# Kernel tuning notes

Measured on AMD Instinct MI355X. Metric: run time of the kernel, lower is better.

## Reference

```python
import jax, jax.numpy as jnp
import numpy as np

B, S, D_IN, D_H, D_OUT, N_LAYERS = 16, 2048, 512, 1024, 10, 2


def setup_inputs() -> dict:
    key = jax.random.key(0)
    ks = jax.random.split(key, 12)
    s = lambda fan_in: 1.0 / np.sqrt(fan_in)
    return {
        "input_vec": jax.random.normal(ks[0], (B, S, D_IN), jnp.float32),
        "game_vector": jax.random.normal(ks[1], (B, N_LAYERS, D_H), jnp.float32),
        "user_vector": jax.random.normal(ks[2], (B, N_LAYERS, D_H), jnp.float32),
        # input_fc: Linear(D_IN, 2*D_IN) -> ReLU -> Linear(2*D_IN, D_H) -> ReLU
        "W1": jax.random.uniform(ks[3], (D_IN, 2 * D_IN), jnp.float32, -s(D_IN), s(D_IN)),
        "b1": jnp.zeros((2 * D_IN,), jnp.float32),
        "W2": jax.random.uniform(ks[4], (2 * D_IN, D_H), jnp.float32, -s(2 * D_IN), s(2 * D_IN)),
        "b2": jnp.zeros((D_H,), jnp.float32),
        # output_fc: Linear(D_H, D_H//2) -> ReLU -> Linear(D_H//2, D_OUT) -> LogSoftmax
        "W3": jax.random.uniform(ks[5], (D_H, D_H // 2), jnp.float32, -s(D_H), s(D_H)),
        "b3": jnp.zeros((D_H // 2,), jnp.float32),
        "W4": jax.random.uniform(ks[6], (D_H // 2, D_OUT), jnp.float32, -s(D_H // 2), s(D_H // 2)),
        "b4": jnp.zeros((D_OUT,), jnp.float32),
    }


def _causal_attention(h):
    # unscaled causal self-attention: softmax(h h^T + triu(-inf)) h
    scores = jnp.einsum("bsd,btd->bst", h, h)  # [B,S,S]
    seq = h.shape[1]
    causal = jnp.tril(jnp.ones((seq, seq), dtype=bool))
    scores = jnp.where(causal[None], scores, -jnp.inf)
    attn = jax.nn.softmax(scores, axis=-1)
    return jnp.einsum("bst,btd->bsd", attn, h)


def reference(input_vec, game_vector, user_vector, W1, b1, W2, b2, W3, b3, W4, b4):
    h = jax.nn.relu(input_vec @ W1 + b1)  # dropout is identity in eval
    h = jax.nn.relu(h @ W2 + b2)          # [B,S,D_H]
    ctx = _causal_attention(h)
    o = jax.nn.relu(ctx @ W3 + b3)
    out = jax.nn.log_softmax(o @ W4 + b4, axis=-1)
    return out, game_vector, user_vector
```

## Files before the change

### kernel.cpp

```cpp
#include <hip/hip_runtime.h>
#include <stdint.h>

#define B_   16
#define S_   2048
#define DIN  512
#define DH   1024
#define DOUT 10

typedef unsigned short u16;
typedef unsigned int   u32;

typedef __bf16 bf16_t;
typedef bf16_t bf16x8 __attribute__((ext_vector_type(8)));
typedef float  f32x4  __attribute__((ext_vector_type(4)));

#define MASKVAL (-3.0e4f)
#define PZ_U16 ((size_t)160 * 16384)

__device__ __forceinline__ float b2f(u16 u) {
    union { u32 i; float f; } v; v.i = ((u32)u) << 16; return v.f;
}
__device__ __forceinline__ u16 f2b(float f) {
    union { float f; u32 i; } v; v.f = f;
    u32 u = v.i;
    u32 r = (u + 0x7FFFu + ((u >> 16) & 1u)) >> 16;
    return (u16)r;
}
__device__ __forceinline__ u32 pack2(float a, float b) {
    return (u32)f2b(a) | ((u32)f2b(b) << 16);
}

__device__ __forceinline__ f32x4 mfma16(bf16x8 a, bf16x8 b, f32x4 c) {
    return __builtin_amdgcn_mfma_f32_16x16x32_bf16(a, b, c, 0, 0, 0);
}

__device__ __forceinline__ void load_lds16(const u16* g, u16* l) {
    __builtin_amdgcn_global_load_lds(
        (__attribute__((address_space(1))) u32*)(g),
        (__attribute__((address_space(3))) u32*)(l), 16, 0, 0);
}

template<bool F32>
__device__ __forceinline__ uint4 ld8(const void* base, size_t eidx) {
    if constexpr (F32) {
        const float* p = (const float*)base + eidx;
        float4 f0 = *(const float4*)p;
        float4 f1 = *(const float4*)(p + 4);
        uint4 r;
        r.x = pack2(f0.x, f0.y); r.y = pack2(f0.z, f0.w);
        r.z = pack2(f1.x, f1.y); r.w = pack2(f1.z, f1.w);
        return r;
    } else {
        return *(const uint4*)((const u16*)base + eidx);
    }
}

__global__ __launch_bounds__(256) void cvt_f32_bf16(
    const float* __restrict__ in, u16* __restrict__ out, int n8)
{
    int i = blockIdx.x * 256 + threadIdx.x;
    if (i >= n8) return;
    size_t e = (size_t)i * 8;
    float4 f0 = *(const float4*)(in + e);
    float4 f1 = *(const float4*)(in + e + 4);
    uint4 r;
    r.x = pack2(f0.x, f0.y); r.y = pack2(f0.z, f0.w);
    r.z = pack2(f1.x, f1.y); r.w = pack2(f1.z, f1.w);
    *(uint4*)(out + e) = r;
}

template<int QR>
__device__ __forceinline__ void rda(bf16x8 (&a)[4][2], const u16* T,
                                    int arow, int quad) {
#pragma unroll
    for (int mf = 0; mf < 4; ++mf) {
        const int row = arow + QR * 64 + mf * 16;
        const int sw = row & 7;
#pragma unroll
        for (int ks = 0; ks < 2; ++ks)
            a[mf][ks] = *(const bf16x8*)(T + row * 64 + (((ks * 4 + quad) ^ sw) << 3));
    }
}

template<int QC>
__device__ __forceinline__ void rdb(bf16x8 (&b)[2][2], const u16* T,
                                    int brow, int quad) {
#pragma unroll
    for (int nf = 0; nf < 2; ++nf) {
        const int row = brow + QC * 128 + nf * 16;
        const int sw = row & 7;
#pragma unroll
        for (int ks = 0; ks < 2; ++ks)
            b[nf][ks] = *(const bf16x8*)(T + row * 64 + (((ks * 4 + quad) ^ sw) << 3));
    }
}

template<int QR, int QC>
__device__ __forceinline__ void mmq(f32x4 (&acc)[2][2][4][2],
                                    const bf16x8 (&a)[4][2],
                                    const bf16x8 (&b)[2][2]) {
#pragma unroll
    for (int ks = 0; ks < 2; ++ks)
#pragma unroll
        for (int mf = 0; mf < 4; ++mf)
#pragma unroll
            for (int nf = 0; nf < 2; ++nf)
                acc[QR][QC][mf][nf] = mfma16(a[mf][ks], b[nf][ks], acc[QR][QC][mf][nf]);
}

#define G8BAR()  __builtin_amdgcn_s_barrier()
#define G8LGKM() do { asm volatile("s_waitcnt lgkmcnt(0)" ::: "memory"); \
                      __builtin_amdgcn_sched_barrier(0); } while (0)
#define G8VMC4() asm volatile("s_waitcnt vmcnt(4)" ::: "memory")

#define G8_LOOP_BODY(NT_)                                                     \
    const int NI = (NT_) >> 1;                                                \
    for (int i = 0; i < NI; ++i) {                                            \
        const int t1 = 2 * i + 1, t2 = 2 * i + 2, t3 = 2 * i + 3;             \
        rda<0>(a, AS_[0], arow, quad); rdb<0>(b0r, BS_[0], brow, quad);       \
        STGB(1, 2, t1); STGB(1, 3, t1);                                       \
        G8BAR(); G8LGKM();                                                    \
        __builtin_amdgcn_s_setprio(1); mmq<0, 0>(acc, a, b0r);                \
        __builtin_amdgcn_s_setprio(0); G8BAR();                               \
        rdb<1>(b1r, BS_[0], brow, quad);                                      \
        STGA(1, 1, t1); STGA(1, 3, t1);                                       \
        G8BAR(); G8LGKM();                                                    \
        __builtin_amdgcn_s_setprio(1); mmq<0, 1>(acc, a, b1r);                \
        __builtin_amdgcn_s_setprio(0); G8BAR();                               \
        rda<1>(a, AS_[0], arow, quad);                                        \
        if (t2 < (NT_)) { STGA(0, 0, t2); STGA(0, 2, t2); }                   \
        G8BAR(); G8LGKM();                                                    \
        __builtin_amdgcn_s_setprio(1); mmq<1, 0>(acc, a, b0r);                \
        __builtin_amdgcn_s_setprio(0); G8BAR();                               \
        if (t2 < (NT_)) { STGB(0, 0, t2); STGB(0, 1, t2); }                   \
        G8BAR();                                                              \
        __builtin_amdgcn_s_setprio(1); mmq<1, 1>(acc, a, b1r);                \
        __builtin_amdgcn_s_setprio(0);                                        \
        G8VMC4(); G8BAR();                                                    \
        rda<0>(a, AS_[1], arow, quad); rdb<0>(b0r, BS_[1], brow, quad);       \
        if (t2 < (NT_)) { STGB(0, 2, t2); STGB(0, 3, t2); }                   \
        G8BAR(); G8LGKM();                                                    \
        __builtin_amdgcn_s_setprio(1); mmq<0, 0>(acc, a, b0r);                \
        __builtin_amdgcn_s_setprio(0); G8BAR();                               \
        rdb<1>(b1r, BS_[1], brow, quad);                                      \
        if (t2 < (NT_)) { STGA(0, 1, t2); STGA(0, 3, t2); }                   \
        G8BAR(); G8LGKM();                                                    \
        __builtin_amdgcn_s_setprio(1); mmq<0, 1>(acc, a, b1r);                \
        __builtin_amdgcn_s_setprio(0); G8BAR();                               \
        rda<1>(a, AS_[1], arow, quad);                                        \
        if (t3 < (NT_)) { STGA(1, 0, t3); STGA(1, 2, t3); }                   \
        G8BAR(); G8LGKM();                                                    \
        __builtin_amdgcn_s_setprio(1); mmq<1, 0>(acc, a, b0r);                \
        __builtin_amdgcn_s_setprio(0); G8BAR();                               \
        if (t3 < (NT_)) { STGB(1, 0, t3); STGB(1, 1, t3); }                   \
        G8BAR();                                                              \
        __builtin_amdgcn_s_setprio(1); mmq<1, 1>(acc, a, b1r);                \
        __builtin_amdgcn_s_setprio(0);                                        \
        G8VMC4(); G8BAR();                                                    \
    }

__global__ __launch_bounds__(512, 2) void gemm8(
    const u16* __restrict__ A, const u16* __restrict__ Bt,
    const float* __restrict__ bias, u16* __restrict__ C,
    int N, int K, int do_relu)
{
    __shared__ __attribute__((aligned(16))) u16 AS_[2][16384];
    __shared__ __attribute__((aligned(16))) u16 BS_[2][16384];

    const int tid  = threadIdx.x;
    const int lane = tid & 63;
    const int w    = tid >> 6;
    const int wm   = w >> 2, wn = w & 3;
    const int quad = lane >> 4, l15 = lane & 15;
    const int m0 = blockIdx.x * 256, n0 = blockIdx.y * 256;

    const int rg = tid >> 3;
    const int ch = (lane & 7) ^ ((lane >> 3) & 7);
    const u16* gA = A  + (size_t)(m0 + rg) * K + ch * 8;
    const u16* gB = Bt + (size_t)(n0 + rg) * K + ch * 8;
    const int wslot = w * 512;

#define STGA(BUF, U, T) load_lds16(gA + (size_t)(U) * 64 * K + (T) * 64, \
                                   &AS_[BUF][(U) * 4096 + wslot])
#define STGB(BUF, U, T) load_lds16(gB + (size_t)(U) * 64 * K + (T) * 64, \
                                   &BS_[BUF][(U) * 4096 + wslot])

    f32x4 acc[2][2][4][2];
#pragma unroll
    for (int p = 0; p < 2; ++p)
#pragma unroll
    for (int q = 0; q < 2; ++q)
#pragma unroll
    for (int m = 0; m < 4; ++m)
#pragma unroll
    for (int n = 0; n < 2; ++n) acc[p][q][m][n] = (f32x4){0.f, 0.f, 0.f, 0.f};

    bf16x8 a[4][2], b0r[2][2], b1r[2][2];

    const int NT = K >> 6;

    STGA(0, 0, 0); STGA(0, 1, 0); STGA(0, 2, 0); STGA(0, 3, 0);
    STGB(0, 0, 0); STGB(0, 1, 0); STGB(0, 2, 0); STGB(0, 3, 0);
    STGA(1, 0, 1); STGA(1, 2, 1);
    STGB(1, 0, 1); STGB(1, 1, 1);
    G8VMC4(); G8BAR();

    const int arow = wm * 128 + l15;
    const int brow = wn * 32 + l15;
    G8_LOOP_BODY(NT)
#undef STGA
#undef STGB

    const int r0 = quad * 4;
#pragma unroll
    for (int qc = 0; qc < 2; ++qc)
#pragma unroll
    for (int nf = 0; nf < 2; ++nf) {
        const int col = n0 + qc * 128 + wn * 32 + nf * 16 + l15;
        const float bv = bias[col];
#pragma unroll
        for (int qr = 0; qr < 2; ++qr)
#pragma unroll
        for (int mf = 0; mf < 4; ++mf) {
            const int rowb = m0 + wm * 128 + qr * 64 + mf * 16 + r0;
#pragma unroll
            for (int r = 0; r < 4; ++r) {
                float v = acc[qr][qc][mf][nf][r] + bv;
                if (do_relu) v = fmaxf(v, 0.f);
                C[(size_t)(rowb + r) * N + col] = f2b(v);
            }
        }
    }
}

__global__ __launch_bounds__(512, 2) void score8(
    const u16* __restrict__ h, u16* __restrict__ P)
{
    __shared__ __attribute__((aligned(16))) u16 AS_[2][16384];
    __shared__ __attribute__((aligned(16))) u16 BS_[2][16384];

    const int z = blockIdx.x / 38;
    const int t = blockIdx.x % 38;

    if (t >= 36) {
        const int p = t - 36;
        const u16 mb = f2b(MASKVAL);
        const u32 m2 = (u32)mb | ((u32)mb << 16);
        uint4 mv; mv.x = m2; mv.y = m2; mv.z = m2; mv.w = m2;
        u16* Pz0 = P + (size_t)z * PZ_U16;
#pragma unroll
        for (int i = 0; i < 8; ++i) {
            const int idx = p * 8 + i;
            const int g  = idx >> 2;
            const int mi = 4 * g + ((idx >> 1) & 1);
            const int ni = 4 * g + 2 + (idx & 1);
            u16* Pz = Pz0 + (size_t)(4 * (g + 1) * (mi - 2 * g)) * 16384;
            const size_t rstride = (size_t)(4 * (g + 1)) * 128;
            for (int q = threadIdx.x; q < 2048; q += 512) {
                int row = q >> 4, cl = (q & 15) * 8;
                *(uint4*)&Pz[(size_t)row * rstride + ni * 128 + cl] = mv;
            }
        }
        return;
    }

    int bi = 0;
    while ((bi + 1) * (bi + 2) / 2 <= t) ++bi;
    const int bj = t - bi * (bi + 1) / 2;
    const bool diag = (bi == bj);

    const int tid  = threadIdx.x;
    const int lane = tid & 63;
    const int w    = tid >> 6;
    const int wm   = w >> 2, wn = w & 3;
    const int quad = lane >> 4, l15 = lane & 15;
    const int m0 = bi * 256, n0 = bj * 256;

    const u16* hz = h + (size_t)z * S_ * DH;
    const int rg = tid >> 3;
    const int ch = (lane & 7) ^ ((lane >> 3) & 7);
    const u16* gA = hz + (size_t)(m0 + rg) * DH + ch * 8;
    const u16* gB = hz + (size_t)(n0 + rg) * DH + ch * 8;
    const int wslot = w * 512;

#define STGA(BUF, U, T) load_lds16(gA + (size_t)(U) * 64 * DH + (T) * 64, \
                                   &AS_[BUF][(U) * 4096 + wslot])
#define STGB(BUF, U, T) load_lds16(gB + (size_t)(U) * 64 * DH + (T) * 64, \
                                   &BS_[BUF][(U) * 4096 + wslot])

    f32x4 acc[2][2][4][2];
#pragma unroll
    for (int p = 0; p < 2; ++p)
#pragma unroll
    for (int q = 0; q < 2; ++q)
#pragma unroll
    for (int m = 0; m < 4; ++m)
#pragma unroll
    for (int n = 0; n < 2; ++n) acc[p][q][m][n] = (f32x4){0.f, 0.f, 0.f, 0.f};

    bf16x8 a[4][2], b0r[2][2], b1r[2][2];

    const int NT = DH >> 6;

    STGA(0, 0, 0); STGA(0, 1, 0); STGA(0, 2, 0); STGA(0, 3, 0);
    STGB(0, 0, 0); STGB(0, 1, 0); STGB(0, 2, 0); STGB(0, 3, 0);
    STGA(1, 0, 1); STGA(1, 2, 1);
    STGB(1, 0, 1); STGB(1, 1, 1);
    G8VMC4(); G8BAR();

    const int arow = wm * 128 + l15;
    const int brow = wn * 32 + l15;
    G8_LOOP_BODY(NT)
#undef STGA
#undef STGB

    const int mi = 2 * bi + wm;
    const int g  = mi >> 2;
    u16* Pz = P + (size_t)z * PZ_U16
                + (size_t)(4 * (g + 1) * (mi - 2 * g)) * 16384;
    const size_t rstride = (size_t)(4 * (g + 1)) * 128;

    const int r0 = quad * 4;
#pragma unroll
    for (int qc = 0; qc < 2; ++qc) {
        const int ni = 2 * bj + qc;
#pragma unroll
        for (int nf = 0; nf < 2; ++nf) {
            const int cl = wn * 32 + nf * 16 + l15;
            const int colg = n0 + qc * 128 + cl;
#pragma unroll
            for (int qr = 0; qr < 2; ++qr)
#pragma unroll
            for (int mf = 0; mf < 4; ++mf) {
                const int rl = qr * 64 + mf * 16 + r0;
                const int rowg = m0 + wm * 128 + rl;
#pragma unroll
                for (int r = 0; r < 4; ++r) {
                    float v = acc[qr][qc][mf][nf][r];
                    if (diag && colg > rowg + r) v = MASKVAL;
                    Pz[(size_t)(rl + r) * rstride + ni * 128 + cl] = f2b(v);
                }
            }
        }
    }
}

__global__ __launch_bounds__(512, 2) void pv8(
    const u16* __restrict__ P, const u16* __restrict__ hT,
    u16* __restrict__ ctx, int nb)
{
    __shared__ __attribute__((aligned(16))) u16 AS_[2][16384];
    __shared__ __attribute__((aligned(16))) u16 BS_[2][16384];

    const int per_bi = 4 * nb;
    const int bi  = 7 - (int)(blockIdx.x / per_bi);
    const int rem = blockIdx.x % per_bi;
    const int nj  = rem & 3;
    const int z   = rem >> 2;

    const int g  = bi >> 1;
    const int K  = (g + 1) * 512;
    const int NT = K >> 6;
    const int n0 = nj * 256;

    const u16* Az = P + (size_t)z * PZ_U16
                      + (size_t)(4 * (g + 1) * (2 * bi - 2 * g)) * 16384;
    const u16* Bz = hT + (size_t)z * DH * S_;
    u16*       C  = ctx + (size_t)z * S_ * DH;

    const int tid  = threadIdx.x;
    const int lane = tid & 63;
    const int w    = tid >> 6;
    const int wm   = w >> 2, wn = w & 3;
    const int quad = lane >> 4, l15 = lane & 15;

    const int rg = tid >> 3;
    const int ch = (lane & 7) ^ ((lane >> 3) & 7);
    const u16* gA = Az + (size_t)rg * K + ch * 8;
    const u16* gB = Bz + (size_t)(n0 + rg) * S_ + ch * 8;
    const int wslot = w * 512;

#define STGA(BUF, U, T) load_lds16(gA + (size_t)(U) * 64 * K + (T) * 64, \
                                   &AS_[BUF][(U) * 4096 + wslot])
#define STGB(BUF, U, T) load_lds16(gB + (size_t)(U) * 64 * S_ + (T) * 64, \
                                   &BS_[BUF][(U) * 4096 + wslot])

    f32x4 acc[2][2][4][2];
#pragma unroll
    for (int p = 0; p < 2; ++p)
#pragma unroll
    for (int q = 0; q < 2; ++q)
#pragma unroll
    for (int m = 0; m < 4; ++m)
#pragma unroll
    for (int n = 0; n < 2; ++n) acc[p][q][m][n] = (f32x4){0.f, 0.f, 0.f, 0.f};

    bf16x8 a[4][2], b0r[2][2], b1r[2][2];

    STGA(0, 0, 0); STGA(0, 1, 0); STGA(0, 2, 0); STGA(0, 3, 0);
    STGB(0, 0, 0); STGB(0, 1, 0); STGB(0, 2, 0); STGB(0, 3, 0);
    STGA(1, 0, 1); STGA(1, 2, 1);
    STGB(1, 0, 1); STGB(1, 1, 1);
    G8VMC4(); G8BAR();

    const int arow = wm * 128 + l15;
    const int brow = wn * 32 + l15;
    G8_LOOP_BODY(NT)
#undef STGA
#undef STGB

    const int r0 = quad * 4;
#pragma unroll
    for (int qc = 0; qc < 2; ++qc)
#pragma unroll
    for (int nf = 0; nf < 2; ++nf) {
        const int col = n0 + qc * 128 + wn * 32 + nf * 16 + l15;
#pragma unroll
        for (int qr = 0; qr < 2; ++qr)
#pragma unroll
        for (int mf = 0; mf < 4; ++mf) {
            const int rowb = bi * 256 + wm * 128 + qr * 64 + mf * 16 + r0;
#pragma unroll
            for (int r = 0; r < 4; ++r)
                C[(size_t)(rowb + r) * DH + col] = f2b(acc[qr][qc][mf][nf][r]);
        }
    }
}

__global__ __launch_bounds__(256) void score_a(
    const u16* __restrict__ h, u16* __restrict__ P)
{
    __shared__ __attribute__((aligned(16))) u16 As[128 * 32];
    __shared__ __attribute__((aligned(16))) u16 Bs[128 * 32];

    const int mi = 15 - blockIdx.x;
    const int ni = blockIdx.y;
    const int g  = mi >> 2;
    const int r4 = (g + 1) * 4;
    if (ni >= r4) return;

    const int tid = threadIdx.x;
    u16* Pz = P + (size_t)blockIdx.z * PZ_U16
                + (size_t)(4 * (g + 1) * (mi - 2 * g)) * 16384;
    const size_t rstride = (size_t)r4 * 128;

    if (ni > mi) {
        const u16 mb = f2b(MASKVAL);
        const u32 m2 = (u32)mb | ((u32)mb << 16);
        uint4 mv; mv.x = m2; mv.y = m2; mv.z = m2; mv.w = m2;
#pragma unroll
        for (int i = 0; i < 8; ++i) {
            int q = tid + i * 256;
            int row = q >> 4, cl = (q & 15) * 8;
            *(uint4*)&Pz[(size_t)row * rstride + ni * 128 + cl] = mv;
        }
        return;
    }

    const int m0 = mi * 128, n0 = ni * 128;
    const u16* A = h + (size_t)blockIdx.z * S_ * DH;

    const int lane = tid & 63;
    const int w    = tid >> 6;
    const int wm   = w >> 1, wn = w & 1;
    const int quad = lane >> 4, l15 = lane & 15;

    const int c0 = tid, c1 = tid + 256;
    const u16* gA0 = A + ((size_t)(m0 + (c0 >> 2)) * DH + (c0 & 3) * 8);
    const u16* gA1 = A + ((size_t)(m0 + (c1 >> 2)) * DH + (c1 & 3) * 8);
    const u16* gB0 = A + ((size_t)(n0 + (c0 >> 2)) * DH + (c0 & 3) * 8);
    const u16* gB1 = A + ((size_t)(n0 + (c1 >> 2)) * DH + (c1 & 3) * 8);
    u16* lA0 = &As[(w * 64) * 8];
    u16* lA1 = &As[(256 + w * 64) * 8];
    u16* lB0 = &Bs[(w * 64) * 8];
    u16* lB1 = &Bs[(256 + w * 64) * 8];

    f32x4 acc[4][4];
#pragma unroll
    for (int i = 0; i < 4; ++i)
#pragma unroll
        for (int j = 0; j < 4; ++j) acc[i][j] = (f32x4){0.f, 0.f, 0.f, 0.f};

    const int nk = DH >> 5;
    for (int kk = 0; kk < nk; ++kk) {
        load_lds16(gA0, lA0); load_lds16(gA1, lA1);
        load_lds16(gB0, lB0); load_lds16(gB1, lB1);
        gA0 += 32; gA1 += 32; gB0 += 32; gB1 += 32;
        __syncthreads();
        bf16x8 af[4], bfr[4];
#pragma unroll
        for (int i = 0; i < 4; ++i)
            af[i] = *(const bf16x8*)&As[(wm * 64 + i * 16 + l15) * 32 + quad * 8];
#pragma unroll
        for (int j = 0; j < 4; ++j)
            bfr[j] = *(const bf16x8*)&Bs[(wn * 64 + j * 16 + l15) * 32 + quad * 8];
#pragma unroll
        for (int i = 0; i < 4; ++i)
#pragma unroll
            for (int j = 0; j < 4; ++j)
                acc[i][j] = mfma16(af[i], bfr[j], acc[i][j]);
        __syncthreads();
    }

    const int r0 = quad * 4;
#pragma unroll
    for (int j = 0; j < 4; ++j) {
        int cl = wn * 64 + j * 16 + l15;
#pragma unroll
        for (int i = 0; i < 4; ++i) {
            int rl = wm * 64 + i * 16 + r0;
#pragma unroll
            for (int r = 0; r < 4; ++r) {
                int row = rl + r;
                float v = (n0 + cl <= m0 + row) ? acc[i][j][r] : MASKVAL;
                Pz[(size_t)row * rstride + ni * 128 + cl] = f2b(v);
            }
        }
    }
}

__global__ __launch_bounds__(256) void softmax_rows(u16* __restrict__ P)
{
    const int tid = threadIdx.x;
    const int lane = tid & 63, w = tid >> 6;
    const size_t row = (size_t)blockIdx.x * 4 + w;
    const int z    = (int)(row >> 11);
    const int rloc = (int)(row & (S_ - 1));
    const int mi = rloc >> 7, g = mi >> 2;
    const int kb = g + 1;
    u16* p = P + (size_t)z * PZ_U16
               + (size_t)(4 * (g + 1) * (mi - 2 * g)) * 16384
               + (size_t)(rloc & 127) * ((g + 1) * 4 * 128);
    float v[32];
    float m = -1e30f;
    for (int k = 0; k < kb; ++k) {
        uint4 u = *(const uint4*)&p[k * 512 + lane * 8];
        const u32* uu = (const u32*)&u;
#pragma unroll
        for (int i = 0; i < 4; ++i) {
            float a = b2f((u16)(uu[i] & 0xFFFFu));
            float b = b2f((u16)(uu[i] >> 16));
            v[k * 8 + 2 * i] = a; v[k * 8 + 2 * i + 1] = b;
            m = fmaxf(m, fmaxf(a, b));
        }
    }
#pragma unroll
    for (int off = 32; off >= 1; off >>= 1) m = fmaxf(m, __shfl_xor(m, off, 64));
    float s = 0.f;
    for (int k = 0; k < kb; ++k)
#pragma unroll
        for (int i = 0; i < 8; ++i) {
            float e = __expf(v[k * 8 + i] - m);
            v[k * 8 + i] = e; s += e;
        }
#pragma unroll
    for (int off = 32; off >= 1; off >>= 1) s += __shfl_xor(s, off, 64);
    float inv = 1.0f / s;
    for (int k = 0; k < kb; ++k) {
        uint4 u; u32* uu = (u32*)&u;
#pragma unroll
        for (int i = 0; i < 4; ++i)
            uu[i] = pack2(v[k * 8 + 2 * i] * inv, v[k * 8 + 2 * i + 1] * inv);
        *(uint4*)&p[k * 512 + lane * 8] = u;
    }
}

__global__ __launch_bounds__(256) void pv_a(
    const u16* __restrict__ P, const u16* __restrict__ hT, u16* __restrict__ ctx,
    int nb)
{
    __shared__ __attribute__((aligned(16))) u16 As[128 * 32];
    __shared__ __attribute__((aligned(16))) u16 Bs[128 * 32];

    const int idx = blockIdx.x;
    const int per_mi = 8 * nb;
    const int mi = 15 - (idx / per_mi);
    const int sub = idx % per_mi;
    const int nblk = sub & 7;
    const int z    = sub >> 3;
    const int g = mi >> 2;
    const int m0 = mi * 128;
    const int n0 = nblk * 128;
    const size_t rstride = (size_t)((g + 1) * 4) * 128;
    const u16* A  = P  + (size_t)z * PZ_U16
                       + (size_t)(4 * (g + 1) * (mi - 2 * g)) * 16384;
    const u16* Bt = hT + (size_t)z * DH * S_;
    u16*      C   = ctx + (size_t)z * S_ * DH;

    const int tid  = threadIdx.x;
    const int lane = tid & 63;
    const int w    = tid >> 6;
    const int wm   = w >> 1, wn = w & 1;
    const int quad = lane >> 4, l15 = lane & 15;

    const int c0 = tid, c1 = tid + 256;
    const u16* gA0 = A  + ((size_t)(c0 >> 2) * rstride + (c0 & 3) * 8);
    const u16* gA1 = A  + ((size_t)(c1 >> 2) * rstride + (c1 & 3) * 8);
    const u16* gB0 = Bt + ((size_t)(n0 + (c0 >> 2)) * S_ + (c0 & 3) * 8);
    const u16* gB1 = Bt + ((size_t)(n0 + (c1 >> 2)) * S_ + (c1 & 3) * 8);
    u16* lA0 = &As[(w * 64) * 8];
    u16* lA1 = &As[(256 + w * 64) * 8];
    u16* lB0 = &Bs[(w * 64) * 8];
    u16* lB1 = &Bs[(256 + w * 64) * 8];

    f32x4 acc[4][4];
#pragma unroll
    for (int i = 0; i < 4; ++i)
#pragma unroll
        for (int j = 0; j < 4; ++j) acc[i][j] = (f32x4){0.f, 0.f, 0.f, 0.f};

    const int nk = (mi + 1) * 4;
    for (int kk = 0; kk < nk; ++kk) {
        load_lds16(gA0, lA0); load_lds16(gA1, lA1);
        load_lds16(gB0, lB0); load_lds16(gB1, lB1);
        gA0 += 32; gA1 += 32; gB0 += 32; gB1 += 32;
        __syncthreads();
        bf16x8 af[4], bfr[4];
#pragma unroll
        for (int i = 0; i < 4; ++i)
            af[i] = *(const bf16x8*)&As[(wm * 64 + i * 16 + l15) * 32 + quad * 8];
#pragma unroll
        for (int j = 0; j < 4; ++j)
            bfr[j] = *(const bf16x8*)&Bs[(wn * 64 + j * 16 + l15) * 32 + quad * 8];
#pragma unroll
        for (int i = 0; i < 4; ++i)
#pragma unroll
            for (int j = 0; j < 4; ++j)
                acc[i][j] = mfma16(af[i], bfr[j], acc[i][j]);
        __syncthreads();
    }

    const int r0 = quad * 4;
#pragma unroll
    for (int j = 0; j < 4; ++j) {
        int col = n0 + wn * 64 + j * 16 + l15;
#pragma unroll
        for (int i = 0; i < 4; ++i) {
            int rowb = m0 + wm * 64 + i * 16 + r0;
#pragma unroll
            for (int r = 0; r < 4; ++r)
                C[(size_t)(rowb + r) * DH + col] = f2b(acc[i][j][r]);
        }
    }
}

template<bool AF32>
__global__ __launch_bounds__(256) void gemm_bt_bias_relu(
    const void* __restrict__ A, const u16* __restrict__ Bt,
    const float* __restrict__ bias, u16* __restrict__ C,
    int M, int N, int K, int do_relu)
{
    __shared__ __attribute__((aligned(16))) u16 As[128 * 32];
    __shared__ __attribute__((aligned(16))) u16 Bs[128 * 32];

    const int tid  = threadIdx.x;
    const int lane = tid & 63;
    const int w    = tid >> 6;
    const int wm   = w >> 1, wn = w & 1;
    const int quad = lane >> 4, l15 = lane & 15;

    const int m0 = blockIdx.x * 128;
    const int n0 = blockIdx.y * 128;

    const int c0 = tid, c1 = tid + 256;
    size_t eA0 = (size_t)(m0 + (c0 >> 2)) * K + (c0 & 3) * 8;
    size_t eA1 = (size_t)(m0 + (c1 >> 2)) * K + (c1 & 3) * 8;
    size_t eB0 = (size_t)(n0 + (c0 >> 2)) * K + (c0 & 3) * 8;
    size_t eB1 = (size_t)(n0 + (c1 >> 2)) * K + (c1 & 3) * 8;

    f32x4 acc[4][4];
#pragma unroll
    for (int i = 0; i < 4; ++i)
#pragma unroll
        for (int j = 0; j < 4; ++j) acc[i][j] = (f32x4){0.f, 0.f, 0.f, 0.f};

    uint4 va0 = ld8<AF32>(A, eA0), va1 = ld8<AF32>(A, eA1);
    uint4 vb0 = ld8<false>(Bt, eB0), vb1 = ld8<false>(Bt, eB1);

    const int nk = K >> 5;
    for (int kk = 0; kk < nk; ++kk) {
        __syncthreads();
        *(uint4*)&As[c0 * 8] = va0;
        *(uint4*)&As[c1 * 8] = va1;
        *(uint4*)&Bs[c0 * 8] = vb0;
        *(uint4*)&Bs[c1 * 8] = vb1;
        if (kk + 1 < nk) {
            eA0 += 32; eA1 += 32; eB0 += 32; eB1 += 32;
            va0 = ld8<AF32>(A, eA0); va1 = ld8<AF32>(A, eA1);
            vb0 = ld8<false>(Bt, eB0); vb1 = ld8<false>(Bt, eB1);
        }
        __syncthreads();
        bf16x8 af[4], bfr[4];
#pragma unroll
        for (int i = 0; i < 4; ++i)
            af[i] = *(const bf16x8*)&As[(wm * 64 + i * 16 + l15) * 32 + quad * 8];
#pragma unroll
        for (int j = 0; j < 4; ++j)
            bfr[j] = *(const bf16x8*)&Bs[(wn * 64 + j * 16 + l15) * 32 + quad * 8];
#pragma unroll
        for (int i = 0; i < 4; ++i)
#pragma unroll
            for (int j = 0; j < 4; ++j)
                acc[i][j] = mfma16(af[i], bfr[j], acc[i][j]);
    }

    const int r0 = quad * 4;
#pragma unroll
    for (int j = 0; j < 4; ++j) {
        int col = n0 + wn * 64 + j * 16 + l15;
        float bv = bias[col];
#pragma unroll
        for (int i = 0; i < 4; ++i) {
            int rowb = m0 + wm * 64 + i * 16 + r0;
#pragma unroll
            for (int r = 0; r < 4; ++r) {
                float v = acc[i][j][r] + bv;
                if (do_relu) v = fmaxf(v, 0.f);
                C[(size_t)(rowb + r) * N + col] = f2b(v);
            }
        }
    }
}

__global__ __launch_bounds__(256) void transpose_cvt(
    const float* __restrict__ in, u16* __restrict__ out, int R, int C)
{
    __shared__ u16 t[32][33];
    int c0 = blockIdx.x * 32, r0 = blockIdx.y * 32;
    int tx = threadIdx.x, ty = threadIdx.y;
#pragma unroll
    for (int i = 0; i < 4; ++i)
        t[ty + i * 8][tx] = f2b(in[(size_t)(r0 + ty + i * 8) * C + c0 + tx]);
    __syncthreads();
#pragma unroll
    for (int i = 0; i < 4; ++i)
        out[(size_t)(c0 + ty + i * 8) * R + r0 + tx] = t[tx][ty + i * 8];
}

__global__ __launch_bounds__(256) void transpose_b(
    const u16* __restrict__ in, u16* __restrict__ out, int R, int C)
{
    __shared__ u16 t[32][33];
    const u16* ip = in  + (size_t)blockIdx.z * R * C;
    u16*       op = out + (size_t)blockIdx.z * R * C;
    int c0 = blockIdx.x * 32, r0 = blockIdx.y * 32;
    int tx = threadIdx.x, ty = threadIdx.y;
#pragma unroll
    for (int i = 0; i < 4; ++i)
        t[ty + i * 8][tx] = ip[(size_t)(r0 + ty + i * 8) * C + c0 + tx];
    __syncthreads();
#pragma unroll
    for (int i = 0; i < 4; ++i)
        op[(size_t)(c0 + ty + i * 8) * R + r0 + tx] = t[tx][ty + i * 8];
}

__global__ __launch_bounds__(256) void head_logsoftmax(
    const u16* __restrict__ o, const float* __restrict__ W4,
    const float* __restrict__ b4, float* __restrict__ out)
{
    __shared__ float W4s[DIN * DOUT];
    __shared__ float b4s[DOUT];
    const int tid = threadIdx.x;
    for (int i = tid; i < DIN * DOUT; i += 256) W4s[i] = W4[i];
    if (tid < DOUT) b4s[tid] = b4[tid];
    __syncthreads();
    const int lane = tid & 63, w = tid >> 6;
    const size_t row = (size_t)blockIdx.x * 4 + w;
    const uint4 ov = *(const uint4*)&o[row * DIN + lane * 8];
    const u32* ou = (const u32*)&ov;
    float oc[8];
#pragma unroll
    for (int i = 0; i < 4; ++i) {
        oc[2*i]   = b2f((u16)(ou[i] & 0xFFFFu));
        oc[2*i+1] = b2f((u16)(ou[i] >> 16));
    }
    float acc[DOUT];
#pragma unroll
    for (int c = 0; c < DOUT; ++c) acc[c] = 0.f;
#pragma unroll
    for (int i = 0; i < 8; ++i) {
        int k = lane * 8 + i;
        float x = oc[i];
#pragma unroll
        for (int c = 0; c < DOUT; ++c) acc[c] += x * W4s[k * DOUT + c];
    }
#pragma unroll
    for (int off = 32; off >= 1; off >>= 1)
#pragma unroll
        for (int c = 0; c < DOUT; ++c) acc[c] += __shfl_xor(acc[c], off, 64);
    float mx = -1e30f;
#pragma unroll
    for (int c = 0; c < DOUT; ++c) { acc[c] += b4s[c]; mx = fmaxf(mx, acc[c]); }
    float sum = 0.f;
#pragma unroll
    for (int c = 0; c < DOUT; ++c) sum += __expf(acc[c] - mx);
    float lse = mx + logf(sum);
    if (lane == 0) {
#pragma unroll
        for (int c = 0; c < DOUT; ++c) out[row * DOUT + c] = acc[c] - lse;
    }
}

extern "C" void kernel_launch(void* const* d_in, const int* in_sizes, int n_in,
                              void* d_out, int out_size, void* d_ws, size_t ws_size,
                              hipStream_t stream) {
    const float* x  = (const float*)d_in[0];
    const float* gv = (const float*)d_in[1];
    const float* uv = (const float*)d_in[2];
    const float* W1 = (const float*)d_in[3];
    const float* b1 = (const float*)d_in[4];
    const float* W2 = (const float*)d_in[5];
    const float* b2 = (const float*)d_in[6];
    const float* W3 = (const float*)d_in[7];
    const float* b3 = (const float*)d_in[8];
    const float* W4 = (const float*)d_in[9];
    const float* b4 = (const float*)d_in[10];
    float* out = (float*)d_out;

    char* ws = (char*)d_ws;
    const size_t MB64 = (size_t)67108864;
    const size_t MiB  = (size_t)1048576;
    const size_t TIER_A3 = 2 * MB64 + 80 * MiB + 4 * MiB;
    const size_t TIER_A2 = 2 * MB64 + 72 * MiB + 8 * MiB;
    const size_t TIER_B  = 3 * MB64 + 5 * MiB;

    if (ws_size >= TIER_A3) {
        u16* h1  = (u16*)(ws);
        u16* hT  = h1;
        u16* h   = (u16*)(ws + MB64);
        u16* ctx = h;
        u16* xb  = (u16*)(ws + 2 * MB64);
        u16* P   = xb;
        u16* o   = xb;
        u16* W1t = (u16*)(ws + 2 * MB64 + 80 * MiB);
        u16* W2t = W1t + 512 * 1024;
        u16* W3t = W2t + 1024 * 1024;

        cvt_f32_bf16<<<8192, 256, 0, stream>>>(x, xb, 2097152);
        transpose_cvt<<<dim3(32, 16), dim3(32, 8), 0, stream>>>(W1, W1t, 512, 1024);
        transpose_cvt<<<dim3(32, 32), dim3(32, 8), 0, stream>>>(W2, W2t, 1024, 1024);
        transpose_cvt<<<dim3(16, 32), dim3(32, 8), 0, stream>>>(W3, W3t, 1024, 512);

        gemm8<<<dim3(128, 4), 512, 0, stream>>>(xb, W1t, b1, h1, 1024, 512, 1);
        gemm8<<<dim3(128, 4), 512, 0, stream>>>(h1, W2t, b2, h,  1024, 1024, 1);

        transpose_b<<<dim3(32, 64, 16), dim3(32, 8), 0, stream>>>(h, hT, 2048, 1024);
        score8<<<38 * 16, 512, 0, stream>>>(h, P);
        softmax_rows<<<8192, 256, 0, stream>>>(P);
        pv8<<<32 * 16, 512, 0, stream>>>(P, hT, ctx, 16);

        gemm8<<<dim3(128, 2), 512, 0, stream>>>(ctx, W3t, b3, o, 512, 1024, 1);
        head_logsoftmax<<<8192, 256, 0, stream>>>(o, W4, b4, out);
    } else if (ws_size >= TIER_A2) {
        u16* h1   = (u16*)(ws);
        u16* ctx  = h1;
        u16* h    = (u16*)(ws + MB64);
        u16* o    = h;
        u16* xb   = (u16*)(ws + 2 * MB64);
        u16* hT_c = xb;
        u16* P_c  = (u16*)(ws + 2 * MB64 + 32 * MiB);
        u16* W1t  = (u16*)(ws + 2 * MB64 + 72 * MiB);
        u16* W2t  = W1t + 512 * 1024;
        u16* W3t  = W2t + 1024 * 1024;

        cvt_f32_bf16<<<8192, 256, 0, stream>>>(x, xb, 2097152);
        transpose_cvt<<<dim3(32, 16), dim3(32, 8), 0, stream>>>(W1, W1t, 512, 1024);
        transpose_cvt<<<dim3(32, 32), dim3(32, 8), 0, stream>>>(W2, W2t, 1024, 1024);
        transpose_cvt<<<dim3(16, 32), dim3(32, 8), 0, stream>>>(W3, W3t, 1024, 512);

        gemm8<<<dim3(128, 4), 512, 0, stream>>>(xb, W1t, b1, h1, 1024, 512, 1);
        gemm8<<<dim3(128, 4), 512, 0, stream>>>(h1, W2t, b2, h,  1024, 1024, 1);

        for (int c = 0; c < 2; ++c) {
            const u16* hc  = h   + (size_t)c * 8 * S_ * DH;
            u16*       cxc = ctx + (size_t)c * 8 * S_ * DH;
            transpose_b<<<dim3(32, 64, 8), dim3(32, 8), 0, stream>>>(hc, hT_c, 2048, 1024);
            score8<<<38 * 8, 512, 0, stream>>>(hc, P_c);
            softmax_rows<<<4096, 256, 0, stream>>>(P_c);
            pv_a<<<16 * 8 * 8, 256, 0, stream>>>(P_c, hT_c, cxc, 8);
        }

        gemm8<<<dim3(128, 2), 512, 0, stream>>>(ctx, W3t, b3, o, 512, 1024, 1);
        head_logsoftmax<<<8192, 256, 0, stream>>>(o, W4, b4, out);
    } else if (ws_size >= TIER_B) {
        u16* h1   = (u16*)(ws);
        u16* ctx  = h1;
        u16* h    = (u16*)(ws + MB64);
        u16* xb   = (u16*)(ws + 2 * MB64);
        u16* hT_c = xb;
        u16* P_c  = (u16*)(ws + 2 * MB64 + 16 * MiB);
        u16* o    = (u16*)(ws + 2 * MB64);
        u16* W1t  = (u16*)(ws + 3 * MB64);
        u16* W2t  = W1t + 512 * 1024;
        u16* W3t  = W2t + 1024 * 1024;

        cvt_f32_bf16<<<8192, 256, 0, stream>>>(x, xb, 2097152);
        transpose_cvt<<<dim3(32, 16), dim3(32, 8), 0, stream>>>(W1, W1t, 512, 1024);
        transpose_cvt<<<dim3(32, 32), dim3(32, 8), 0, stream>>>(W2, W2t, 1024, 1024);
        transpose_cvt<<<dim3(16, 32), dim3(32, 8), 0, stream>>>(W3, W3t, 1024, 512);

        gemm8<<<dim3(128, 4), 512, 0, stream>>>(xb, W1t, b1, h1, 1024, 512, 1);
        gemm8<<<dim3(128, 4), 512, 0, stream>>>(h1, W2t, b2, h,  1024, 1024, 1);

        for (int c = 0; c < 4; ++c) {
            const u16* hc  = h   + (size_t)c * 4 * S_ * DH;
            u16*       cxc = ctx + (size_t)c * 4 * S_ * DH;
            transpose_b<<<dim3(32, 64, 4), dim3(32, 8), 0, stream>>>(hc, hT_c, 2048, 1024);
            score8<<<38 * 4, 512, 0, stream>>>(hc, P_c);
            softmax_rows<<<2048, 256, 0, stream>>>(P_c);
            pv_a<<<16 * 8 * 4, 256, 0, stream>>>(P_c, hT_c, cxc, 4);
        }

        gemm8<<<dim3(128, 2), 512, 0, stream>>>(ctx, W3t, b3, o, 512, 1024, 1);
        head_logsoftmax<<<8192, 256, 0, stream>>>(o, W4, b4, out);
    } else {
        u16* h    = (u16*)(ws);
        u16* hT_b = (u16*)(ws + MB64);
        u16* P_b  = (u16*)(ws + MB64 + 4 * MiB);
        u16* ctx_b= (u16*)(ws + MB64 + 12 * MiB);
        u16* o_b  = (u16*)(ws + MB64 + 16 * MiB);
        u16* W1t  = (u16*)(ws + MB64 + 18 * MiB);
        u16* W2t  = W1t + 512 * 1024;
        u16* W3t  = W2t + 1024 * 1024;
        u16* h1_b = P_b;

        transpose_cvt<<<dim3(32, 16), dim3(32, 8), 0, stream>>>(W1, W1t, 512, 1024);
        transpose_cvt<<<dim3(32, 32), dim3(32, 8), 0, stream>>>(W2, W2t, 1024, 1024);
        transpose_cvt<<<dim3(16, 32), dim3(32, 8), 0, stream>>>(W3, W3t, 1024, 512);

        for (int c = 0; c < 8; ++c) {
            const float* xc = x + (size_t)c * 4096 * DIN;
            u16*         hc = h + (size_t)c * 4096 * DH;
            gemm_bt_bias_relu<true ><<<dim3(32, 8), 256, 0, stream>>>(xc, W1t, b1, h1_b,
                                                                      4096, 1024, 512, 1);
            gemm_bt_bias_relu<false><<<dim3(32, 8), 256, 0, stream>>>(h1_b, W2t, b2, hc,
                                                                      4096, 1024, 1024, 1);
        }
        for (int b = 0; b < B_; ++b) {
            const u16* hb = h + (size_t)b * S_ * DH;
            transpose_b<<<dim3(32, 64, 1), dim3(32, 8), 0, stream>>>(hb, hT_b, 2048, 1024);
            score_a<<<dim3(16, 16, 1), 256, 0, stream>>>(hb, P_b);
            softmax_rows<<<512, 256, 0, stream>>>(P_b);
            pv_a<<<16 * 8, 256, 0, stream>>>(P_b, hT_b, ctx_b, 1);
            gemm_bt_bias_relu<false><<<dim3(16, 4), 256, 0, stream>>>(ctx_b, W3t, b3, o_b,
                                                                      2048, 512, 1024, 1);
            head_logsoftmax<<<512, 256, 0, stream>>>(o_b, W4, b4,
                                                     out + (size_t)b * S_ * DOUT);
        }
    }

    size_t n_gv = (size_t)in_sizes[1], n_uv = (size_t)in_sizes[2];
    size_t o0 = (size_t)out_size - n_gv - n_uv;
    hipMemcpyAsync(out + o0,        gv, n_gv * 4, hipMemcpyDeviceToDevice, stream);
    hipMemcpyAsync(out + o0 + n_gv, uv, n_uv * 4, hipMemcpyDeviceToDevice, stream);
}
```

Measured before the change: 588.4 us.

## Vectorize h transpose, merge weight prep, XCD-remap score blocks, batch head rows

Several independent tweaks. The three weight transpose-convert launches are merged into one wprep kernel. The bf16 h transpose now uses 16-byte vector loads and stores over 64x32 tiles. score8 remaps block indices so blocks of the same batch land on the same XCD when the batch count is a multiple of eight. head_logsoftmax processes four rows per wave, so it launches a quarter as many blocks and amortizes its W4 shared-memory load. The aim is fewer launches, better memory coalescing and better L2 locality, at the cost of more bank conflicts in the new transpose's shared-memory access pattern.

```diff
diff --git a/kernel.cpp b/kernel.cpp
--- a/kernel.cpp
+++ b/kernel.cpp
@@ -234,13 +234,20 @@
 }
 
 __global__ __launch_bounds__(512, 2) void score8(
-    const u16* __restrict__ h, u16* __restrict__ P)
+    const u16* __restrict__ h, u16* __restrict__ P, int nbb)
 {
     __shared__ __attribute__((aligned(16))) u16 AS_[2][16384];
     __shared__ __attribute__((aligned(16))) u16 BS_[2][16384];
 
-    const int z = blockIdx.x / 38;
-    const int t = blockIdx.x % 38;
+    int z, t;
+    if ((nbb & 7) == 0) {
+        const int xcd = blockIdx.x & 7, slot = blockIdx.x >> 3;
+        z = (slot / 38) * 8 + xcd;
+        t = slot % 38;
+    } else {
+        z = blockIdx.x / 38;
+        t = blockIdx.x % 38;
+    }
 
     if (t >= 36) {
         const int p = t - 36;
@@ -722,36 +729,51 @@
     }
 }
 
-__global__ __launch_bounds__(256) void transpose_cvt(
-    const float* __restrict__ in, u16* __restrict__ out, int R, int C)
+__global__ __launch_bounds__(256) void wprep(
+    const float* __restrict__ W1, const float* __restrict__ W2,
+    const float* __restrict__ W3,
+    u16* __restrict__ W1t, u16* __restrict__ W2t, u16* __restrict__ W3t)
 {
     __shared__ u16 t[32][33];
-    int c0 = blockIdx.x * 32, r0 = blockIdx.y * 32;
-    int tx = threadIdx.x, ty = threadIdx.y;
-#pragma unroll
-    for (int i = 0; i < 4; ++i)
-        t[ty + i * 8][tx] = f2b(in[(size_t)(r0 + ty + i * 8) * C + c0 + tx]);
+    int i = blockIdx.x;
+    const float* in; u16* out; int R, C, xt;
+    if (i < 512)       { in = W1; out = W1t; R = 512;  C = 1024; xt = 32; }
+    else if (i < 1536) { in = W2; out = W2t; R = 1024; C = 1024; xt = 32; i -= 512; }
+    else               { in = W3; out = W3t; R = 1024; C = 512;  xt = 16; i -= 1536; }
+    const int c0 = (i % xt) * 32, r0 = (i / xt) * 32;
+    const int tx = threadIdx.x, ty = threadIdx.y;
+#pragma unroll
+    for (int k = 0; k < 4; ++k)
+        t[ty + k * 8][tx] = f2b(in[(size_t)(r0 + ty + k * 8) * C + c0 + tx]);
     __syncthreads();
 #pragma unroll
-    for (int i = 0; i < 4; ++i)
-        out[(size_t)(c0 + ty + i * 8) * R + r0 + tx] = t[tx][ty + i * 8];
-}
-
-__global__ __launch_bounds__(256) void transpose_b(
+    for (int k = 0; k < 4; ++k)
+        out[(size_t)(c0 + ty + k * 8) * R + r0 + tx] = t[tx][ty + k * 8];
+}
+
+__global__ __launch_bounds__(256) void transpose_v(
     const u16* __restrict__ in, u16* __restrict__ out, int R, int C)
 {
-    __shared__ u16 t[32][33];
+    __shared__ u16 st[64][33];
     const u16* ip = in  + (size_t)blockIdx.z * R * C;
     u16*       op = out + (size_t)blockIdx.z * R * C;
-    int c0 = blockIdx.x * 32, r0 = blockIdx.y * 32;
-    int tx = threadIdx.x, ty = threadIdx.y;
-#pragma unroll
-    for (int i = 0; i < 4; ++i)
-        t[ty + i * 8][tx] = ip[(size_t)(r0 + ty + i * 8) * C + c0 + tx];
+    const int c0 = blockIdx.x * 64, r0 = blockIdx.y * 32;
+    const int t = threadIdx.x;
+    {
+        const int row = t >> 3, ch = t & 7;
+        uint4 v = *(const uint4*)&ip[(size_t)(r0 + row) * C + c0 + ch * 8];
+        const u16* pv = (const u16*)&v;
+#pragma unroll
+        for (int k = 0; k < 8; ++k) st[ch * 8 + k][row] = pv[k];
+    }
     __syncthreads();
-#pragma unroll
-    for (int i = 0; i < 4; ++i)
-        op[(size_t)(c0 + ty + i * 8) * R + r0 + tx] = t[tx][ty + i * 8];
+    {
+        const int oc = t >> 2, r4 = t & 3;
+        uint4 v; u16* pv = (u16*)&v;
+#pragma unroll
+        for (int k = 0; k < 8; ++k) pv[k] = st[oc][r4 * 8 + k];
+        *(uint4*)&op[(size_t)(c0 + oc) * R + r0 + r4 * 8] = v;
+    }
 }
 
 __global__ __launch_bounds__(256) void head_logsoftmax(
@@ -765,39 +787,41 @@
     if (tid < DOUT) b4s[tid] = b4[tid];
     __syncthreads();
     const int lane = tid & 63, w = tid >> 6;
-    const size_t row = (size_t)blockIdx.x * 4 + w;
-    const uint4 ov = *(const uint4*)&o[row * DIN + lane * 8];
-    const u32* ou = (const u32*)&ov;
-    float oc[8];
-#pragma unroll
-    for (int i = 0; i < 4; ++i) {
-        oc[2*i]   = b2f((u16)(ou[i] & 0xFFFFu));
-        oc[2*i+1] = b2f((u16)(ou[i] >> 16));
-    }
-    float acc[DOUT];
-#pragma unroll
-    for (int c = 0; c < DOUT; ++c) acc[c] = 0.f;
-#pragma unroll
-    for (int i = 0; i < 8; ++i) {
-        int k = lane * 8 + i;
-        float x = oc[i];
-#pragma unroll
-        for (int c = 0; c < DOUT; ++c) acc[c] += x * W4s[k * DOUT + c];
-    }
-#pragma unroll
-    for (int off = 32; off >= 1; off >>= 1)
-#pragma unroll
-        for (int c = 0; c < DOUT; ++c) acc[c] += __shfl_xor(acc[c], off, 64);
-    float mx = -1e30f;
-#pragma unroll
-    for (int c = 0; c < DOUT; ++c) { acc[c] += b4s[c]; mx = fmaxf(mx, acc[c]); }
-    float sum = 0.f;
-#pragma unroll
-    for (int c = 0; c < DOUT; ++c) sum += __expf(acc[c] - mx);
-    float lse = mx + logf(sum);
-    if (lane == 0) {
-#pragma unroll
-        for (int c = 0; c < DOUT; ++c) out[row * DOUT + c] = acc[c] - lse;
+    for (int rr = 0; rr < 4; ++rr) {
+        const size_t row = (size_t)blockIdx.x * 16 + w * 4 + rr;
+        const uint4 ov = *(const uint4*)&o[row * DIN + lane * 8];
+        const u32* ou = (const u32*)&ov;
+        float oc[8];
+#pragma unroll
+        for (int i = 0; i < 4; ++i) {
+            oc[2*i]   = b2f((u16)(ou[i] & 0xFFFFu));
+            oc[2*i+1] = b2f((u16)(ou[i] >> 16));
+        }
+        float acc[DOUT];
+#pragma unroll
+        for (int c = 0; c < DOUT; ++c) acc[c] = 0.f;
+#pragma unroll
+        for (int i = 0; i < 8; ++i) {
+            int k = lane * 8 + i;
+            float x = oc[i];
+#pragma unroll
+            for (int c = 0; c < DOUT; ++c) acc[c] += x * W4s[k * DOUT + c];
+        }
+#pragma unroll
+        for (int off = 32; off >= 1; off >>= 1)
+#pragma unroll
+            for (int c = 0; c < DOUT; ++c) acc[c] += __shfl_xor(acc[c], off, 64);
+        float mx = -1e30f;
+#pragma unroll
+        for (int c = 0; c < DOUT; ++c) { acc[c] += b4s[c]; mx = fmaxf(mx, acc[c]); }
+        float sum = 0.f;
+#pragma unroll
+        for (int c = 0; c < DOUT; ++c) sum += __expf(acc[c] - mx);
+        float lse = mx + logf(sum);
+        if (lane == 0) {
+#pragma unroll
+            for (int c = 0; c < DOUT; ++c) out[row * DOUT + c] = acc[c] - lse;
+        }
     }
 }
 
@@ -837,20 +861,18 @@
         u16* W3t = W2t + 1024 * 1024;
 
         cvt_f32_bf16<<<8192, 256, 0, stream>>>(x, xb, 2097152);
-        transpose_cvt<<<dim3(32, 16), dim3(32, 8), 0, stream>>>(W1, W1t, 512, 1024);
-        transpose_cvt<<<dim3(32, 32), dim3(32, 8), 0, stream>>>(W2, W2t, 1024, 1024);
-        transpose_cvt<<<dim3(16, 32), dim3(32, 8), 0, stream>>>(W3, W3t, 1024, 512);
+        wprep<<<2048, dim3(32, 8), 0, stream>>>(W1, W2, W3, W1t, W2t, W3t);
 
         gemm8<<<dim3(128, 4), 512, 0, stream>>>(xb, W1t, b1, h1, 1024, 512, 1);
         gemm8<<<dim3(128, 4), 512, 0, stream>>>(h1, W2t, b2, h,  1024, 1024, 1);
 
-        transpose_b<<<dim3(32, 64, 16), dim3(32, 8), 0, stream>>>(h, hT, 2048, 1024);
-        score8<<<38 * 16, 512, 0, stream>>>(h, P);
+        transpose_v<<<dim3(16, 64, 16), 256, 0, stream>>>(h, hT, 2048, 1024);
+        score8<<<38 * 16, 512, 0, stream>>>(h, P, 16);
         softmax_rows<<<8192, 256, 0, stream>>>(P);
         pv8<<<32 * 16, 512, 0, stream>>>(P, hT, ctx, 16);
 
         gemm8<<<dim3(128, 2), 512, 0, stream>>>(ctx, W3t, b3, o, 512, 1024, 1);
-        head_logsoftmax<<<8192, 256, 0, stream>>>(o, W4, b4, out);
+        head_logsoftmax<<<2048, 256, 0, stream>>>(o, W4, b4, out);
     } else if (ws_size >= TIER_A2) {
         u16* h1   = (u16*)(ws);
         u16* ctx  = h1;
@@ -864,9 +886,7 @@
         u16* W3t  = W2t + 1024 * 1024;
 
         cvt_f32_bf16<<<8192, 256, 0, stream>>>(x, xb, 2097152);
-        transpose_cvt<<<dim3(32, 16), dim3(32, 8), 0, stream>>>(W1, W1t, 512, 1024);
-        transpose_cvt<<<dim3(32, 32), dim3(32, 8), 0, stream>>>(W2, W2t, 1024, 1024);
-        transpose_cvt<<<dim3(16, 32), dim3(32, 8), 0, stream>>>(W3, W3t, 1024, 512);
+        wprep<<<2048, dim3(32, 8), 0, stream>>>(W1, W2, W3, W1t, W2t, W3t);
 
         gemm8<<<dim3(128, 4), 512, 0, stream>>>(xb, W1t, b1, h1, 1024, 512, 1);
         gemm8<<<dim3(128, 4), 512, 0, stream>>>(h1, W2t, b2, h,  1024, 1024, 1);
@@ -874,14 +894,14 @@
         for (int c = 0; c < 2; ++c) {
             const u16* hc  = h   + (size_t)c * 8 * S_ * DH;
             u16*       cxc = ctx + (size_t)c * 8 * S_ * DH;
-            transpose_b<<<dim3(32, 64, 8), dim3(32, 8), 0, stream>>>(hc, hT_c, 2048, 1024);
-            score8<<<38 * 8, 512, 0, stream>>>(hc, P_c);
+            transpose_v<<<dim3(16, 64, 8), 256, 0, stream>>>(hc, hT_c, 2048, 1024);
+            score8<<<38 * 8, 512, 0, stream>>>(hc, P_c, 8);
             softmax_rows<<<4096, 256, 0, stream>>>(P_c);
             pv_a<<<16 * 8 * 8, 256, 0, stream>>>(P_c, hT_c, cxc, 8);
         }
 
         gemm8<<<dim3(128, 2), 512, 0, stream>>>(ctx, W3t, b3, o, 512, 1024, 1);
-        head_logsoftmax<<<8192, 256, 0, stream>>>(o, W4, b4, out);
+        head_logsoftmax<<<2048, 256, 0, stream>>>(o, W4, b4, out);
     } else if (ws_size >= TIER_B) {
         u16* h1   = (u16*)(ws);
         u16* ctx  = h1;
@@ -895,9 +915,7 @@
         u16* W3t  = W2t + 1024 * 1024;
 
         cvt_f32_bf16<<<8192, 256, 0, stream>>>(x, xb, 2097152);
-        transpose_cvt<<<dim3(32, 16), dim3(32, 8), 0, stream>>>(W1, W1t, 512, 1024);
-        transpose_cvt<<<dim3(32, 32), dim3(32, 8), 0, stream>>>(W2, W2t, 1024, 1024);
-        transpose_cvt<<<dim3(16, 32), dim3(32, 8), 0, stream>>>(W3, W3t, 1024, 512);
+        wprep<<<2048, dim3(32, 8), 0, stream>>>(W1, W2, W3, W1t, W2t, W3t);
 
         gemm8<<<dim3(128, 4), 512, 0, stream>>>(xb, W1t, b1, h1, 1024, 512, 1);
         gemm8<<<dim3(128, 4), 512, 0, stream>>>(h1, W2t, b2, h,  1024, 1024, 1);
@@ -905,14 +923,14 @@
         for (int c = 0; c < 4; ++c) {
             const u16* hc  = h   + (size_t)c * 4 * S_ * DH;
             u16*       cxc = ctx + (size_t)c * 4 * S_ * DH;
-            transpose_b<<<dim3(32, 64, 4), dim3(32, 8), 0, stream>>>(hc, hT_c, 2048, 1024);
-            score8<<<38 * 4, 512, 0, stream>>>(hc, P_c);
+            transpose_v<<<dim3(16, 64, 4), 256, 0, stream>>>(hc, hT_c, 2048, 1024);
+            score8<<<38 * 4, 512, 0, stream>>>(hc, P_c, 4);
             softmax_rows<<<2048, 256, 0, stream>>>(P_c);
             pv_a<<<16 * 8 * 4, 256, 0, stream>>>(P_c, hT_c, cxc, 4);
         }
 
         gemm8<<<dim3(128, 2), 512, 0, stream>>>(ctx, W3t, b3, o, 512, 1024, 1);
-        head_logsoftmax<<<8192, 256, 0, stream>>>(o, W4, b4, out);
+        head_logsoftmax<<<2048, 256, 0, stream>>>(o, W4, b4, out);
     } else {
         u16* h    = (u16*)(ws);
         u16* hT_b = (u16*)(ws + MB64);
@@ -924,9 +942,7 @@
         u16* W3t  = W2t + 1024 * 1024;
         u16* h1_b = P_b;
 
-        transpose_cvt<<<dim3(32, 16), dim3(32, 8), 0, stream>>>(W1, W1t, 512, 1024);
-        transpose_cvt<<<dim3(32, 32), dim3(32, 8), 0, stream>>>(W2, W2t, 1024, 1024);
-        transpose_cvt<<<dim3(16, 32), dim3(32, 8), 0, stream>>>(W3, W3t, 1024, 512);
+        wprep<<<2048, dim3(32, 8), 0, stream>>>(W1, W2, W3, W1t, W2t, W3t);
 
         for (int c = 0; c < 8; ++c) {
             const float* xc = x + (size_t)c * 4096 * DIN;
@@ -938,13 +954,13 @@
         }
         for (int b = 0; b < B_; ++b) {
             const u16* hb = h + (size_t)b * S_ * DH;
-            transpose_b<<<dim3(32, 64, 1), dim3(32, 8), 0, stream>>>(hb, hT_b, 2048, 1024);
+            transpose_v<<<dim3(16, 64, 1), 256, 0, stream>>>(hb, hT_b, 2048, 1024);
             score_a<<<dim3(16, 16, 1), 256, 0, stream>>>(hb, P_b);
             softmax_rows<<<512, 256, 0, stream>>>(P_b);
             pv_a<<<16 * 8, 256, 0, stream>>>(P_b, hT_b, ctx_b, 1);
             gemm_bt_bias_relu<false><<<dim3(16, 4), 256, 0, stream>>>(ctx_b, W3t, b3, o_b,
                                                                       2048, 512, 1024, 1);
-            head_logsoftmax<<<512, 256, 0, stream>>>(o_b, W4, b4,
+            head_logsoftmax<<<128, 256, 0, stream>>>(o_b, W4, b4,
                                                      out + (size_t)b * S_ * DOUT);
         }
     }
```

Result: faster. 548.6 us (-6.8%).
